# Kernel tuning notes

Measured on AMD Instinct MI355X. Metric: run time of the kernel, lower is better.

## Reference

```python
import jax, jax.numpy as jnp
import numpy as np

# Config constants matching init_kwargs (layer_no=2 -> stride 8, anch_mask=[0,1,2])
ANCHORS = np.array([[10,13],[16,30],[33,23],[30,61],[62,45],[59,119],
                    [116,90],[156,198],[373,326]], np.float32)
STRIDE = 8.0
N_CLASSES = 80
A = 3          # n_anchors in this head
IGNORE = 0.7   # ignore_thre
LAMBDA = 0.5


def _forward(xin, labels, W, b):
    B = xin.shape[0]
    F = xin.shape[2]
    n_ch = 5 + N_CLASSES
    anchors = jnp.asarray(ANCHORS) / STRIDE      # all_anchors_grid, [9,2]
    m_anch = anchors[:A]                         # masked_anchors (anch_mask=[0,1,2])

    # 1x1 conv -> [B, A, F, F, n_ch]
    out = jnp.einsum('bchw,oc->bohw', xin, W) + b[None, :, None, None]
    out = out.reshape(B, A, n_ch, F, F).transpose(0, 1, 3, 4, 2)
    ch = jnp.arange(n_ch)
    output = jnp.where((ch < 2) | (ch >= 4), jax.nn.sigmoid(out), out)

    # box decode (pred); only [..., :4] is used (detached) for IoU ignore mask
    xs = jnp.arange(F, dtype=xin.dtype)
    pred_x = output[..., 0] + xs                 # x varies along last spatial axis
    pred_y = output[..., 1] + xs[:, None]        # y varies along rows
    pred_w = jnp.exp(output[..., 2]) * m_anch[:, 0][None, :, None, None]
    pred_h = jnp.exp(output[..., 3]) * m_anch[:, 1][None, :, None, None]
    pred4 = jax.lax.stop_gradient(jnp.stack([pred_x, pred_y, pred_w, pred_h], -1))

    lab = jax.lax.stop_gradient(labels)          # original uses labels.cpu().data
    valid = lab.sum(-1) > 0                      # [B,K]
    tx = lab[..., 1] * F
    ty = lab[..., 2] * F
    tw = lab[..., 3] * F
    th = lab[..., 4] * F
    ti = tx.astype(jnp.int32)
    tj = ty.astype(jnp.int32)
    tbox = jnp.stack([tx, ty, tw, th], -1)       # [B,K,4]

    # anchor matching: bboxes_iou(truth_box, ref_anchors) with xyxy=True, faithful to source
    ref = jnp.concatenate([jnp.zeros_like(anchors), anchors], -1)   # [9,4] = [0,0,w,h]
    tl = jnp.maximum(tbox[..., None, :2], ref[:, :2])
    br = jnp.minimum(tbox[..., None, 2:], ref[:, 2:])
    area_a = jnp.prod(tbox[..., 2:] - tbox[..., :2], -1)            # [B,K]
    area_b = anchors[:, 0] * anchors[:, 1]                          # [9]
    ai = jnp.prod(br - tl, -1) * jnp.all(tl < br, -1)
    a_iou = ai / (area_a[..., None] + area_b - ai)                  # [B,K,9]
    a_iou = jnp.where(valid[..., None], a_iou, -1.0)
    best_all = jnp.argmax(a_iou, -1)                                # [B,K]
    best_mask = best_all < A                                        # in anch_mask {0,1,2}
    best_n = best_all % A

    # pred-vs-truth IoU (xywh) -> objectness ignore mask
    p = pred4.reshape(B, -1, 4)                                     # [B, A*F*F, 4]
    ptl = p[..., :2] - p[..., 2:] * 0.5
    pbr = p[..., :2] + p[..., 2:] * 0.5
    ttl = tbox[..., :2] - tbox[..., 2:] * 0.5
    tbr = tbox[..., :2] + tbox[..., 2:] * 0.5
    tl2 = jnp.maximum(ptl[:, :, None], ttl[:, None])                # [B,N,K,2]
    br2 = jnp.minimum(pbr[:, :, None], tbr[:, None])
    ai2 = jnp.prod(br2 - tl2, -1) * jnp.all(tl2 < br2, -1)
    denom = (p[..., 2] * p[..., 3])[:, :, None] + (tbox[..., 2] * tbox[..., 3])[:, None, :] - ai2
    piou = jnp.where(valid[:, None, :], ai2 / denom, 0.0)
    obj_mask = 1.0 - (piou.max(-1) > IGNORE).astype(xin.dtype).reshape(B, A, F, F)

    # vectorized scatter of per-truth-box assignments
    assign = valid & best_mask
    bidx = jnp.broadcast_to(jnp.arange(B)[:, None], valid.shape)
    lin = ((bidx * A + best_n) * F + tj) * F + ti
    ncells = B * A * F * F
    lin = jnp.where(assign, lin, ncells).reshape(-1)    # OOB rows dropped in scatter

    aw = m_anch[best_n, 0]
    ah = m_anch[best_n, 1]
    onehot = jax.nn.one_hot(lab[..., 0].astype(jnp.int32), N_CLASSES, dtype=xin.dtype)
    tvec = jnp.concatenate([
        (tx - ti)[..., None], (ty - tj)[..., None],
        jnp.log(tw / aw + 1e-16)[..., None], jnp.log(th / ah + 1e-16)[..., None],
        jnp.ones_like(tx)[..., None], onehot], -1).reshape(-1, n_ch)
    scale = jnp.sqrt(2.0 - tw * th / (F * F))           # [B,K]

    obj_mask = obj_mask.reshape(-1).at[lin].set(1.0, mode='drop').reshape(B, A, F, F)
    tgt_mask = jnp.zeros((ncells, 4 + N_CLASSES), xin.dtype).at[lin].set(1.0, mode='drop')
    tgt_mask = tgt_mask.reshape(B, A, F, F, 4 + N_CLASSES)
    tgt_scale = jnp.zeros((ncells, 2), xin.dtype).at[lin].set(
        jnp.stack([scale, scale], -1).reshape(-1, 2), mode='drop').reshape(B, A, F, F, 2)
    target = jnp.zeros((ncells, n_ch), xin.dtype).at[lin].set(tvec, mode='drop')
    target = target.reshape(B, A, F, F, n_ch)

    def process(x):
        xy = x[..., :2] * tgt_mask[..., :2]
        wh = x[..., 2:4] * tgt_mask[..., 2:4] * tgt_scale
        obj = (x[..., 4] * obj_mask)[..., None]
        cl = x[..., 5:] * tgt_mask[..., 4:]
        return jnp.concatenate([xy, wh, obj, cl], -1)

    o = process(output)
    t = process(target)

    def bce(p_, t_, w=None):
        # torch BCELoss clamps log terms at -100
        l = -(t_ * jnp.maximum(jnp.log(p_), -100.0)
              + (1.0 - t_) * jnp.maximum(jnp.log(1.0 - p_), -100.0))
        return (l * w if w is not None else l).sum()

    loss_xy = bce(o[..., :2], t[..., :2], tgt_scale * tgt_scale)
    loss_wh = LAMBDA * ((o[..., 2:4] - t[..., 2:4]) ** 2).sum()
    loss_obj = bce(o[..., 4], t[..., 4])
    loss_cls = bce(o[..., 5:], t[..., 5:])
    loss_l2 = ((o - t) ** 2).sum()
    loss = loss_xy + loss_wh + loss_obj + loss_cls
    return jnp.stack([loss, loss_xy, loss_wh, loss_obj, loss_cls, loss_l2])


def setup_inputs() -> dict:
    key = jax.random.key(0)
    k1, k2, k3, k4, k5 = jax.random.split(key, 5)
    B, C, F, K = 16, 256, 76, 40
    n_ch = 5 + N_CLASSES
    xin = jax.random.normal(k1, (B, C, F, F), jnp.float32)
    W = jax.random.normal(k2, (A * n_ch, C), jnp.float32) * 0.02  # 1x1 conv weight
    b = jnp.zeros((A * n_ch,), jnp.float32)
    cls = jax.random.randint(k3, (B, K, 1), 0, N_CLASSES).astype(jnp.float32)
    xy = jax.random.uniform(k4, (B, K, 2), jnp.float32, 0.05, 0.95)
    wh = jax.random.uniform(k5, (B, K, 2), jnp.float32, 0.02, 0.4)
    labels = jnp.concatenate([cls, xy, wh], -1)   # [B,K,5] = [class,xc,yc,w,h]
    return {"xin": xin, "labels": labels, "W": W, "b": b}


def reference(xin, labels, W, b):
    return _forward(xin, labels, W, b)
```

## Files before the change

kernel.cpp:

```cpp
#include <hip/hip_runtime.h>
#include <math.h>

typedef unsigned int u32;
typedef unsigned short u16;
typedef __attribute__((ext_vector_type(2))) u32 u32x2;
typedef __attribute__((ext_vector_type(4))) u32 u32x4;
typedef __attribute__((ext_vector_type(8))) short bf16x8;
typedef __attribute__((ext_vector_type(4))) float f32x4;

#define FDIM 76
#define NCELL 5776
#define NA 3
#define NCH 85
#define NCLS 80
#define KLAB 40
#define NB 16
#define CIN 256
#define TILES_PER_B 91
#define NBLK (NB * TILES_PER_B)
#define CS_LD 68

__device__ __forceinline__ float sigmf_(float x) { return __frcp_rn(1.0f + __expf(-x)); }
__device__ __forceinline__ float bce_fullf(float p, float t) {
    return -(t * fmaxf(__logf(p), -100.0f) + (1.0f - t) * fmaxf(__logf(1.0f - p), -100.0f));
}
__device__ __forceinline__ float bce1f(float p) { return -fmaxf(__logf(p), -100.0f); }
__device__ __forceinline__ float bce0f(float p) { return -fmaxf(__logf(1.0f - p), -100.0f); }

__device__ __forceinline__ u16 bf16rne(float f) {
    u32 u = __float_as_uint(f);
    u32 r = u + 0x7fffu + ((u >> 16) & 1u);
    return (u16)(r >> 16);
}
__device__ __forceinline__ float bf16f(u16 v) { return __uint_as_float(((u32)v) << 16); }

__global__ __launch_bounds__(256) void yolo_wconv(const float* __restrict__ W,
                                                  u16* __restrict__ Wbf) {
    int idx = blockIdx.x * 256 + threadIdx.x;
    int row = idx >> 8, col = idx & 255;
    float v = (row < NA * NCH) ? W[row * CIN + col] : 0.0f;
    Wbf[idx] = bf16rne(v);
}

__global__ __launch_bounds__(64) void yolo_lab(const float* __restrict__ labels,
                                               float* __restrict__ lrec) {
    int idx = blockIdx.x * 64 + threadIdx.x;
    if (idx >= NB * KLAB) return;
    const float* l = labels + idx * 5;
    float cls = l[0], x = l[1], y = l[2], ww = l[3], hh = l[4];
    bool valid = (cls + x + y + ww + hh) > 0.0f;
    float tx = x * FDIM, ty = y * FDIM, tw = ww * FDIM, th = hh * FDIM;
    int ti = (int)tx, tj = (int)ty;
    float area_a = (tw - tx) * (th - ty);
    const float aw[9] = {1.25f, 2.0f, 4.125f, 3.75f, 7.75f, 7.375f, 14.5f, 19.5f, 46.625f};
    const float ah[9] = {1.625f, 3.75f, 2.875f, 7.625f, 5.625f, 14.875f, 11.25f, 24.75f, 40.75f};
    float best = -1e30f;
    int bi = 0;
    for (int n = 0; n < 9; n++) {
        float bw = fminf(tw, aw[n]), bh = fminf(th, ah[n]);
        float ai = ((tx < bw) && (ty < bh)) ? (bw - tx) * (bh - ty) : 0.0f;
        float iou = valid ? ai / (area_a + aw[n] * ah[n] - ai) : -1.0f;
        if (iou > best) { best = iou; bi = n; }
    }
    int bn = bi % 3;
    bool assign = valid && (bi < 3);
    float* r = lrec + idx * 16;
    r[0] = tx - 0.5f * tw; r[1] = ty - 0.5f * th;
    r[2] = tx + 0.5f * tw; r[3] = ty + 0.5f * th;
    r[4] = tw * th;
    r[5] = valid ? 1.0f : 0.0f;
    r[6] = assign ? (float)((bn * FDIM + tj) * FDIM + ti) : -1.0f;
    r[7] = sqrtf(2.0f - tw * th / (float)(FDIM * FDIM));
    r[8] = tx - (float)ti; r[9] = ty - (float)tj;
    r[10] = logf(tw / aw[bn] + 1e-16f); r[11] = logf(th / ah[bn] + 1e-16f);
    r[12] = cls; r[13] = 0.0f; r[14] = 0.0f; r[15] = 0.0f;
}

__global__ __launch_bounds__(512, 4) void yolo_mfma(const float* __restrict__ xin,
                                                    const u16* __restrict__ Wbf,
                                                    const float* __restrict__ bias,
                                                    const float* __restrict__ lrec,
                                                    float* __restrict__ partials) {
    __shared__ char smem[34816];
    __shared__ float Lb[KLAB * 16];
    __shared__ float red[8][8];

    u16* Csb = (u16*)smem;

    const int blk = blockIdx.x;
    const int b = blk / TILES_PER_B;
    const int tile = blk - b * TILES_PER_B;
    const int cell0 = tile * 64;
    const int t = threadIdx.x;
    const int lane = t & 63;
    const int wid = t >> 6;
    const int g = lane >> 4;
    const int l15 = lane & 15;

    const float* xbase = xin + (size_t)b * CIN * NCELL;
    float xv[32];
    {
        const int cell = t & 63;
        const int cg0 = cell0 + cell;
        const int cg = cg0 < NCELL ? cg0 : NCELL - 1;
        const int kq0 = (t >> 6);
#pragma unroll
        for (int kc = 0; kc < 4; kc++)
#pragma unroll
            for (int ii = 0; ii < 2; ii++) {
                const int kq = kq0 + ii * 8;
                const float* xp = xbase + (size_t)(kc * 64 + kq * 4) * NCELL + cg;
                xv[kc * 8 + ii * 4 + 0] = xp[0];
                xv[kc * 8 + ii * 4 + 1] = xp[NCELL];
                xv[kc * 8 + ii * 4 + 2] = xp[2 * NCELL];
                xv[kc * 8 + ii * 4 + 3] = xp[3 * NCELL];
            }
    }

    for (int i = t; i < KLAB * 16; i += 512) Lb[i] = lrec[b * KLAB * 16 + i];

    f32x4 acc[2][4];
#pragma unroll
    for (int mi = 0; mi < 2; mi++)
#pragma unroll
        for (int ni = 0; ni < 4; ni++) acc[mi][ni] = (f32x4){0.f, 0.f, 0.f, 0.f};

    const u16* wrow = Wbf + (wid * 32 + l15) * CIN;

#pragma unroll
    for (int kc = 0; kc < 4; kc++) {
        u16* Xs = (u16*)(smem + ((kc & 1) ? 8192 : 0));
        bf16x8 af0[2];
#pragma unroll
        for (int mi = 0; mi < 2; mi++)
            af0[mi] = *(const bf16x8*)(wrow + mi * 16 * CIN + kc * 64 + g * 8);
#pragma unroll
        for (int ii = 0; ii < 2; ii++) {
            const int u = t + ii * 512;
            const int kq = u >> 6, cell = u & 63;
            u32x2 pv;
            pv.x = (u32)bf16rne(xv[kc * 8 + ii * 4 + 0]) | ((u32)bf16rne(xv[kc * 8 + ii * 4 + 1]) << 16);
            pv.y = (u32)bf16rne(xv[kc * 8 + ii * 4 + 2]) | ((u32)bf16rne(xv[kc * 8 + ii * 4 + 3]) << 16);
            const int byte = (cell * 128 + kq * 8) ^ ((cell & 7) << 4);
            *(u32x2*)((char*)Xs + byte) = pv;
        }
        __syncthreads();
        bf16x8 bfr[4];
#pragma unroll
        for (int ni = 0; ni < 4; ni++) {
            const int cell = ni * 16 + l15;
            const int byte = (cell * 128 + g * 16) ^ ((cell & 7) << 4);
            bfr[ni] = *(const bf16x8*)((char*)Xs + byte);
        }
        bf16x8 af1[2];
#pragma unroll
        for (int mi = 0; mi < 2; mi++)
            af1[mi] = *(const bf16x8*)(wrow + mi * 16 * CIN + kc * 64 + 32 + g * 8);
#pragma unroll
        for (int mi = 0; mi < 2; mi++)
#pragma unroll
            for (int ni = 0; ni < 4; ni++)
                acc[mi][ni] = __builtin_amdgcn_mfma_f32_16x16x32_bf16(
                    af0[mi], bfr[ni], acc[mi][ni], 0, 0, 0);
#pragma unroll
        for (int ni = 0; ni < 4; ni++) {
            const int cell = ni * 16 + l15;
            const int byte = (cell * 128 + 64 + g * 16) ^ ((cell & 7) << 4);
            bfr[ni] = *(const bf16x8*)((char*)Xs + byte);
        }
#pragma unroll
        for (int mi = 0; mi < 2; mi++)
#pragma unroll
            for (int ni = 0; ni < 4; ni++)
                acc[mi][ni] = __builtin_amdgcn_mfma_f32_16x16x32_bf16(
                    af1[mi], bfr[ni], acc[mi][ni], 0, 0, 0);
    }

    __syncthreads();

    float bv[8];
#pragma unroll
    for (int mi = 0; mi < 2; mi++)
#pragma unroll
        for (int reg = 0; reg < 4; reg++) {
            const int ch = wid * 32 + mi * 16 + g * 4 + reg;
            bv[mi * 4 + reg] = (ch < NA * NCH) ? bias[ch] : 0.0f;
        }
#pragma unroll
    for (int mi = 0; mi < 2; mi++)
#pragma unroll
        for (int ni = 0; ni < 4; ni++)
#pragma unroll
            for (int reg = 0; reg < 4; reg++) {
                const int ch = wid * 32 + mi * 16 + g * 4 + reg;
                const int cell = ni * 16 + l15;
                Csb[ch * CS_LD + cell] = bf16rne(acc[mi][ni][reg] + bv[mi * 4 + reg]);
            }
    __syncthreads();

    float part[5] = {0.f, 0.f, 0.f, 0.f, 0.f};
    if (t < 384) {
        const int half = (t >= 192) ? 1 : 0;
        const int unit = t - half * 192;
        const int a = unit >> 6;
        const int c = unit & 63;
        const int cg = cell0 + c;
        if (cg < NCELL) {
            const int chb = a * NCH;
            const int hh = cg / FDIM;
            const int ww = cg - hh * FDIM;
            const float mykey = (float)((a * FDIM + hh) * FDIM + ww);
            if (half == 0) {
                float v0 = bf16f(Csb[(chb + 0) * CS_LD + c]);
                float v1 = bf16f(Csb[(chb + 1) * CS_LD + c]);
                float v2 = bf16f(Csb[(chb + 2) * CS_LD + c]);
                float v3 = bf16f(Csb[(chb + 3) * CS_LD + c]);
                float v4 = bf16f(Csb[(chb + 4) * CS_LD + c]);
                const float manw[3] = {1.25f, 2.0f, 4.125f};
                const float manh[3] = {1.625f, 3.75f, 2.875f};
                float s0 = sigmf_(v0), s1 = sigmf_(v1), s4 = sigmf_(v4);
                float pw = __expf(v2) * manw[a];
                float ph = __expf(v3) * manh[a];
                float px = s0 + (float)ww, py = s1 + (float)hh;
                float parea = pw * ph;
                float ptlx = px - 0.5f * pw, ptly = py - 0.5f * ph;
                float pbrx = px + 0.5f * pw, pbry = py + 0.5f * ph;

                float maxiou = -1e30f;
                int aidx = -1;
                for (int k = 0; k < KLAB; k++) {
                    const f32x4 A = *(const f32x4*)&Lb[k * 16];
                    const f32x4 Bq = *(const f32x4*)&Lb[k * 16 + 4];
                    float tlx = fmaxf(ptlx, A.x), tly = fmaxf(ptly, A.y);
                    float brx = fminf(pbrx, A.z), bry = fminf(pbry, A.w);
                    float inter = ((tlx < brx) && (tly < bry)) ? (brx - tlx) * (bry - tly) : 0.0f;
                    float iou = (Bq.y != 0.0f) ? inter * __frcp_rn(parea + Bq.x - inter) : 0.0f;
                    maxiou = fmaxf(maxiou, iou);
                    if (Bq.z == mykey) aidx = k;
                }
                if (aidx >= 0) {
                    const f32x4 Bq = *(const f32x4*)&Lb[aidx * 16 + 4];
                    const f32x4 Tv = *(const f32x4*)&Lb[aidx * 16 + 8];
                    float sc = Bq.w, sc2 = sc * sc;
                    part[0] += sc2 * (bce_fullf(s0, Tv.x) + bce_fullf(s1, Tv.y));
                    float dw = v2 - Tv.z, dh = v3 - Tv.w;
                    float whq = dw * dw + dh * dh;
                    part[1] += 0.5f * sc2 * whq;
                    part[2] += bce1f(s4);
                    int ci = (int)Lb[aidx * 16 + 12];
                    float l2 = (s0 - Tv.x) * (s0 - Tv.x) + (s1 - Tv.y) * (s1 - Tv.y) +
                               sc2 * whq + (s4 - 1.0f) * (s4 - 1.0f);
                    float lcls = 0.0f;
                    for (int cc = 0; cc < 40; cc++) {
                        float s = sigmf_(bf16f(Csb[(chb + 5 + cc) * CS_LD + c]));
                        if (cc == ci) { lcls += bce1f(s); l2 += (s - 1.0f) * (s - 1.0f); }
                        else          { lcls += bce0f(s); l2 += s * s; }
                    }
                    part[3] += lcls;
                    part[4] += l2;
                } else {
                    bool objm = !(maxiou > 0.7f);
                    if (objm) { part[2] += bce0f(s4); part[4] += s4 * s4; }
                }
            } else {
                int aidx = -1;
                for (int k = 0; k < KLAB; k++) {
                    const f32x4 Bq = *(const f32x4*)&Lb[k * 16 + 4];
                    if (Bq.z == mykey) aidx = k;
                }
                if (aidx >= 0) {
                    int ci = (int)Lb[aidx * 16 + 12];
                    float lcls = 0.0f, l2 = 0.0f;
                    for (int cc = 40; cc < 80; cc++) {
                        float s = sigmf_(bf16f(Csb[(chb + 5 + cc) * CS_LD + c]));
                        if (cc == ci) { lcls += bce1f(s); l2 += (s - 1.0f) * (s - 1.0f); }
                        else          { lcls += bce0f(s); l2 += s * s; }
                    }
                    part[3] += lcls;
                    part[4] += l2;
                }
            }
        }
    }

#pragma unroll
    for (int i = 0; i < 5; i++) {
        float v = part[i];
        for (int off = 32; off > 0; off >>= 1) v += __shfl_down(v, off);
        if ((t & 63) == 0) red[t >> 6][i] = v;
    }
    __syncthreads();
    if (t == 0) {
        float s[5];
#pragma unroll
        for (int i = 0; i < 5; i++) {
            s[i] = red[0][i];
#pragma unroll
            for (int wv = 1; wv < 8; wv++) s[i] += red[wv][i];
            partials[blk * 8 + i] = s[i];
        }
    }
}

__global__ __launch_bounds__(256) void yolo_fin(const float* __restrict__ partials,
                                                float* __restrict__ out) {
    __shared__ float red[4][8];
    const int t = threadIdx.x;
    float s[5] = {0.f, 0.f, 0.f, 0.f, 0.f};
    for (int r = t; r < NBLK; r += 256)
#pragma unroll
        for (int i = 0; i < 5; i++) s[i] += partials[r * 8 + i];
#pragma unroll
    for (int i = 0; i < 5; i++) {
        float v = s[i];
        for (int off = 32; off > 0; off >>= 1) v += __shfl_down(v, off);
        if ((t & 63) == 0) red[t >> 6][i] = v;
    }
    __syncthreads();
    if (t == 0) {
        float xy  = red[0][0] + red[1][0] + red[2][0] + red[3][0];
        float wh  = red[0][1] + red[1][1] + red[2][1] + red[3][1];
        float obj = red[0][2] + red[1][2] + red[2][2] + red[3][2];
        float cls = red[0][3] + red[1][3] + red[2][3] + red[3][3];
        float l2  = red[0][4] + red[1][4] + red[2][4] + red[3][4];
        out[0] = xy + wh + obj + cls;
        out[1] = xy; out[2] = wh; out[3] = obj; out[4] = cls; out[5] = l2;
    }
}

extern "C" void kernel_launch(void* const* d_in, const int* in_sizes, int n_in,
                              void* d_out, int out_size, void* d_ws, size_t ws_size,
                              hipStream_t stream) {
    const float* xin    = (const float*)d_in[0];
    const float* labels = (const float*)d_in[1];
    const float* Wm     = (const float*)d_in[2];
    const float* bias   = (const float*)d_in[3];
    float* out = (float*)d_out;

    float* partials = (float*)d_ws;
    float* lrec  = (float*)((char*)d_ws + 46592);
    u16*   Wbf   = (u16*)((char*)d_ws + 46592 + 40960);

    yolo_wconv<<<256, 256, 0, stream>>>(Wm, Wbf);
    yolo_lab<<<(NB * KLAB + 63) / 64, 64, 0, stream>>>(labels, lrec);
    yolo_mfma<<<NBLK, 512, 0, stream>>>(xin, Wbf, bias, lrec, partials);
    yolo_fin<<<1, 256, 0, stream>>>(partials, out);
}
```

Measured before the change: 86.38 us.

## Split fused GEMM+loss kernel into separate GEMM and loss kernels via global bf16 buffer

Splits the previously fused conv-GEMM-plus-loss kernel into a GEMM kernel that writes bf16 conv outputs to a global workspace buffer and a separate loss kernel where one thread handles each anchor-cell. The aim is to remove load imbalance and the idle threads in the fused epilogue, where only 384 of 512 threads worked and the IoU and label scan serialized behind the GEMM. Global x loads now happen per k-chunk instead of all up front, which lowers register pressure. In exchange it adds about 47 MB of extra global write and read traffic plus an extra launch. The fused kernel is kept as a fallback when the workspace is too small.

Result: slower. 105.4 us (+22.0%).

```diff
diff --git a/kernel.cpp b/kernel.cpp
--- a/kernel.cpp
+++ b/kernel.cpp
@@ -18,6 +18,8 @@
 #define CIN 256
 #define TILES_PER_B 91
 #define NBLK (NB * TILES_PER_B)
+#define LOSS_BLKX 68
+#define NBLK2 (NB * LOSS_BLKX)
 #define CS_LD 68
 
 __device__ __forceinline__ float sigmf_(float x) { return __frcp_rn(1.0f + __expf(-x)); }
@@ -76,14 +78,11 @@
     r[12] = cls; r[13] = 0.0f; r[14] = 0.0f; r[15] = 0.0f;
 }
 
-__global__ __launch_bounds__(512, 4) void yolo_mfma(const float* __restrict__ xin,
+__global__ __launch_bounds__(512, 4) void yolo_gemm(const float* __restrict__ xin,
                                                     const u16* __restrict__ Wbf,
                                                     const float* __restrict__ bias,
-                                                    const float* __restrict__ lrec,
-                                                    float* __restrict__ partials) {
+                                                    u16* __restrict__ Cg) {
     __shared__ char smem[34816];
-    __shared__ float Lb[KLAB * 16];
-    __shared__ float red[8][8];
 
     u16* Csb = (u16*)smem;
 
@@ -97,34 +96,13 @@
     const int g = lane >> 4;
     const int l15 = lane & 15;
 
+    f32x4 acc[2][4];
+#pragma unroll
+    for (int mi = 0; mi < 2; mi++)
+#pragma unroll
+        for (int ni = 0; ni < 4; ni++) acc[mi][ni] = (f32x4){0.f, 0.f, 0.f, 0.f};
+
     const float* xbase = xin + (size_t)b * CIN * NCELL;
-    float xv[32];
-    {
-        const int cell = t & 63;
-        const int cg0 = cell0 + cell;
-        const int cg = cg0 < NCELL ? cg0 : NCELL - 1;
-        const int kq0 = (t >> 6);
-#pragma unroll
-        for (int kc = 0; kc < 4; kc++)
-#pragma unroll
-            for (int ii = 0; ii < 2; ii++) {
-                const int kq = kq0 + ii * 8;
-                const float* xp = xbase + (size_t)(kc * 64 + kq * 4) * NCELL + cg;
-                xv[kc * 8 + ii * 4 + 0] = xp[0];
-                xv[kc * 8 + ii * 4 + 1] = xp[NCELL];
-                xv[kc * 8 + ii * 4 + 2] = xp[2 * NCELL];
-                xv[kc * 8 + ii * 4 + 3] = xp[3 * NCELL];
-            }
-    }
-
-    for (int i = t; i < KLAB * 16; i += 512) Lb[i] = lrec[b * KLAB * 16 + i];
-
-    f32x4 acc[2][4];
-#pragma unroll
-    for (int mi = 0; mi < 2; mi++)
-#pragma unroll
-        for (int ni = 0; ni < 4; ni++) acc[mi][ni] = (f32x4){0.f, 0.f, 0.f, 0.f};
-
     const u16* wrow = Wbf + (wid * 32 + l15) * CIN;
 
 #pragma unroll
@@ -134,13 +112,26 @@
 #pragma unroll
         for (int mi = 0; mi < 2; mi++)
             af0[mi] = *(const bf16x8*)(wrow + mi * 16 * CIN + kc * 64 + g * 8);
+        float xv[8];
+#pragma unroll
+        for (int ii = 0; ii < 2; ii++) {
+            const int u = t + ii * 512;
+            const int kq = u >> 6, cell = u & 63;
+            const int cg0 = cell0 + cell;
+            const int cg = cg0 < NCELL ? cg0 : NCELL - 1;
+            const float* xp = xbase + (size_t)(kc * 64 + kq * 4) * NCELL + cg;
+            xv[ii * 4 + 0] = xp[0];
+            xv[ii * 4 + 1] = xp[NCELL];
+            xv[ii * 4 + 2] = xp[2 * NCELL];
+            xv[ii * 4 + 3] = xp[3 * NCELL];
+        }
 #pragma unroll
         for (int ii = 0; ii < 2; ii++) {
             const int u = t + ii * 512;
             const int kq = u >> 6, cell = u & 63;
             u32x2 pv;
-            pv.x = (u32)bf16rne(xv[kc * 8 + ii * 4 + 0]) | ((u32)bf16rne(xv[kc * 8 + ii * 4 + 1]) << 16);
-            pv.y = (u32)bf16rne(xv[kc * 8 + ii * 4 + 2]) | ((u32)bf16rne(xv[kc * 8 + ii * 4 + 3]) << 16);
+            pv.x = (u32)bf16rne(xv[ii * 4 + 0]) | ((u32)bf16rne(xv[ii * 4 + 1]) << 16);
+            pv.y = (u32)bf16rne(xv[ii * 4 + 2]) | ((u32)bf16rne(xv[ii * 4 + 3]) << 16);
             const int byte = (cell * 128 + kq * 8) ^ ((cell & 7) << 4);
             *(u32x2*)((char*)Xs + byte) = pv;
         }
@@ -198,6 +189,216 @@
             }
     __syncthreads();
 
+    u16* cgb = Cg + (size_t)b * 256 * NCELL;
+#pragma unroll
+    for (int it = 0; it < 16; it++) {
+        const int i = t + it * 512;
+        const int ch = i >> 5;
+        const int cw = i & 31;
+        const int cell = cell0 + cw * 2;
+        if (cell + 2 <= NCELL) {
+            u32 v = *(const u32*)&Csb[ch * CS_LD + cw * 2];
+            *(u32*)&cgb[(size_t)ch * NCELL + cell] = v;
+        }
+    }
+}
+
+__global__ __launch_bounds__(256) void yolo_loss(const u16* __restrict__ Cg,
+                                                 const float* __restrict__ lrec,
+                                                 float* __restrict__ partials) {
+    __shared__ float Lb[KLAB * 16];
+    __shared__ float red[4][8];
+    const int b = blockIdx.y;
+    const int t = threadIdx.x;
+    const int idx = blockIdx.x * 256 + t;
+
+    for (int i = t; i < KLAB * 16; i += 256) Lb[i] = lrec[b * KLAB * 16 + i];
+    __syncthreads();
+
+    float part[5] = {0.f, 0.f, 0.f, 0.f, 0.f};
+    if (idx < NA * NCELL) {
+        int a = 0, cell = idx;
+        if (idx >= 2 * NCELL)      { a = 2; cell = idx - 2 * NCELL; }
+        else if (idx >= NCELL)     { a = 1; cell = idx - NCELL; }
+        const int hh = cell / FDIM;
+        const int ww = cell - hh * FDIM;
+        const float mykey = (float)((a * FDIM + hh) * FDIM + ww);
+        const u16* cp = Cg + (size_t)b * 256 * NCELL + (size_t)(a * NCH) * NCELL + cell;
+
+        float v0 = bf16f(cp[0]);
+        float v1 = bf16f(cp[NCELL]);
+        float v2 = bf16f(cp[2 * NCELL]);
+        float v3 = bf16f(cp[3 * NCELL]);
+        float v4 = bf16f(cp[4 * NCELL]);
+        const float manw[3] = {1.25f, 2.0f, 4.125f};
+        const float manh[3] = {1.625f, 3.75f, 2.875f};
+        float s0 = sigmf_(v0), s1 = sigmf_(v1), s4 = sigmf_(v4);
+        float pw = __expf(v2) * manw[a];
+        float ph = __expf(v3) * manh[a];
+        float px = s0 + (float)ww, py = s1 + (float)hh;
+        float parea = pw * ph;
+        float ptlx = px - 0.5f * pw, ptly = py - 0.5f * ph;
+        float pbrx = px + 0.5f * pw, pbry = py + 0.5f * ph;
+
+        float maxiou = -1e30f;
+        int aidx = -1;
+        for (int k = 0; k < KLAB; k++) {
+            const f32x4 A  = *(const f32x4*)&Lb[k * 16];
+            const f32x4 Bq = *(const f32x4*)&Lb[k * 16 + 4];
+            float tlx = fmaxf(ptlx, A.x), tly = fmaxf(ptly, A.y);
+            float brx = fminf(pbrx, A.z), bry = fminf(pbry, A.w);
+            float inter = ((tlx < brx) && (tly < bry)) ? (brx - tlx) * (bry - tly) : 0.0f;
+            float iou = (Bq.y != 0.0f) ? inter * __frcp_rn(parea + Bq.x - inter) : 0.0f;
+            maxiou = fmaxf(maxiou, iou);
+            if (Bq.z == mykey) aidx = k;
+        }
+        if (aidx >= 0) {
+            const f32x4 Bq = *(const f32x4*)&Lb[aidx * 16 + 4];
+            const f32x4 Tv = *(const f32x4*)&Lb[aidx * 16 + 8];
+            float sc = Bq.w, sc2 = sc * sc;
+            part[0] += sc2 * (bce_fullf(s0, Tv.x) + bce_fullf(s1, Tv.y));
+            float dw = v2 - Tv.z, dh = v3 - Tv.w;
+            float whq = dw * dw + dh * dh;
+            part[1] += 0.5f * sc2 * whq;
+            part[2] += bce1f(s4);
+            int ci = (int)Lb[aidx * 16 + 12];
+            float l2 = (s0 - Tv.x) * (s0 - Tv.x) + (s1 - Tv.y) * (s1 - Tv.y) +
+                       sc2 * whq + (s4 - 1.0f) * (s4 - 1.0f);
+            float lcls = 0.0f;
+#pragma unroll 4
+            for (int cc = 0; cc < NCLS; cc++) {
+                float s = sigmf_(bf16f(cp[(size_t)(5 + cc) * NCELL]));
+                if (cc == ci) { lcls += bce1f(s); l2 += (s - 1.0f) * (s - 1.0f); }
+                else          { lcls += bce0f(s); l2 += s * s; }
+            }
+            part[3] += lcls;
+            part[4] += l2;
+        } else {
+            bool objm = !(maxiou > 0.7f);
+            if (objm) { part[2] += bce0f(s4); part[4] += s4 * s4; }
+        }
+    }
+
+#pragma unroll
+    for (int i = 0; i < 5; i++) {
+        float v = part[i];
+        for (int off = 32; off > 0; off >>= 1) v += __shfl_down(v, off);
+        if ((t & 63) == 0) red[t >> 6][i] = v;
+    }
+    __syncthreads();
+    if (t == 0) {
+#pragma unroll
+        for (int i = 0; i < 5; i++)
+            partials[(b * LOSS_BLKX + blockIdx.x) * 8 + i] =
+                red[0][i] + red[1][i] + red[2][i] + red[3][i];
+    }
+}
+
+__global__ __launch_bounds__(512, 4) void yolo_mfma(const float* __restrict__ xin,
+                                                    const u16* __restrict__ Wbf,
+                                                    const float* __restrict__ bias,
+                                                    const float* __restrict__ lrec,
+                                                    float* __restrict__ partials) {
+    __shared__ char smem[34816];
+    __shared__ float Lb[KLAB * 16];
+    __shared__ float red[8][8];
+    u16* Csb = (u16*)smem;
+    const int blk = blockIdx.x;
+    const int b = blk / TILES_PER_B;
+    const int tile = blk - b * TILES_PER_B;
+    const int cell0 = tile * 64;
+    const int t = threadIdx.x;
+    const int lane = t & 63;
+    const int wid = t >> 6;
+    const int g = lane >> 4;
+    const int l15 = lane & 15;
+
+    for (int i = t; i < KLAB * 16; i += 512) Lb[i] = lrec[b * KLAB * 16 + i];
+
+    f32x4 acc[2][4];
+#pragma unroll
+    for (int mi = 0; mi < 2; mi++)
+#pragma unroll
+        for (int ni = 0; ni < 4; ni++) acc[mi][ni] = (f32x4){0.f, 0.f, 0.f, 0.f};
+    const float* xbase = xin + (size_t)b * CIN * NCELL;
+    const u16* wrow = Wbf + (wid * 32 + l15) * CIN;
+#pragma unroll
+    for (int kc = 0; kc < 4; kc++) {
+        u16* Xs = (u16*)(smem + ((kc & 1) ? 8192 : 0));
+        bf16x8 af0[2];
+#pragma unroll
+        for (int mi = 0; mi < 2; mi++)
+            af0[mi] = *(const bf16x8*)(wrow + mi * 16 * CIN + kc * 64 + g * 8);
+        float xv[8];
+#pragma unroll
+        for (int ii = 0; ii < 2; ii++) {
+            const int u = t + ii * 512;
+            const int kq = u >> 6, cell = u & 63;
+            const int cg0 = cell0 + cell;
+            const int cg = cg0 < NCELL ? cg0 : NCELL - 1;
+            const float* xp = xbase + (size_t)(kc * 64 + kq * 4) * NCELL + cg;
+            xv[ii * 4 + 0] = xp[0]; xv[ii * 4 + 1] = xp[NCELL];
+            xv[ii * 4 + 2] = xp[2 * NCELL]; xv[ii * 4 + 3] = xp[3 * NCELL];
+        }
+#pragma unroll
+        for (int ii = 0; ii < 2; ii++) {
+            const int u = t + ii * 512;
+            const int kq = u >> 6, cell = u & 63;
+            u32x2 pv;
+            pv.x = (u32)bf16rne(xv[ii * 4 + 0]) | ((u32)bf16rne(xv[ii * 4 + 1]) << 16);
+            pv.y = (u32)bf16rne(xv[ii * 4 + 2]) | ((u32)bf16rne(xv[ii * 4 + 3]) << 16);
+            const int byte = (cell * 128 + kq * 8) ^ ((cell & 7) << 4);
+            *(u32x2*)((char*)Xs + byte) = pv;
+        }
+        __syncthreads();
+        bf16x8 bfr[4];
+#pragma unroll
+        for (int ni = 0; ni < 4; ni++) {
+            const int cell = ni * 16 + l15;
+            const int byte = (cell * 128 + g * 16) ^ ((cell & 7) << 4);
+            bfr[ni] = *(const bf16x8*)((char*)Xs + byte);
+        }
+        bf16x8 af1[2];
+#pragma unroll
+        for (int mi = 0; mi < 2; mi++)
+            af1[mi] = *(const bf16x8*)(wrow + mi * 16 * CIN + kc * 64 + 32 + g * 8);
+#pragma unroll
+        for (int mi = 0; mi < 2; mi++)
+#pragma unroll
+            for (int ni = 0; ni < 4; ni++)
+                acc[mi][ni] = __builtin_amdgcn_mfma_f32_16x16x32_bf16(af0[mi], bfr[ni], acc[mi][ni], 0, 0, 0);
+#pragma unroll
+        for (int ni = 0; ni < 4; ni++) {
+            const int cell = ni * 16 + l15;
+            const int byte = (cell * 128 + 64 + g * 16) ^ ((cell & 7) << 4);
+            bfr[ni] = *(const bf16x8*)((char*)Xs + byte);
+        }
+#pragma unroll
+        for (int mi = 0; mi < 2; mi++)
+#pragma unroll
+            for (int ni = 0; ni < 4; ni++)
+                acc[mi][ni] = __builtin_amdgcn_mfma_f32_16x16x32_bf16(af1[mi], bfr[ni], acc[mi][ni], 0, 0, 0);
+    }
+    __syncthreads();
+    float bv[8];
+#pragma unroll
+    for (int mi = 0; mi < 2; mi++)
+#pragma unroll
+        for (int reg = 0; reg < 4; reg++) {
+            const int ch = wid * 32 + mi * 16 + g * 4 + reg;
+            bv[mi * 4 + reg] = (ch < NA * NCH) ? bias[ch] : 0.0f;
+        }
+#pragma unroll
+    for (int mi = 0; mi < 2; mi++)
+#pragma unroll
+        for (int ni = 0; ni < 4; ni++)
+#pragma unroll
+            for (int reg = 0; reg < 4; reg++) {
+                const int ch = wid * 32 + mi * 16 + g * 4 + reg;
+                const int cell = ni * 16 + l15;
+                Csb[ch * CS_LD + cell] = bf16rne(acc[mi][ni][reg] + bv[mi * 4 + reg]);
+            }
+    __syncthreads();
     float part[5] = {0.f, 0.f, 0.f, 0.f, 0.f};
     if (t < 384) {
         const int half = (t >= 192) ? 1 : 0;
@@ -225,7 +426,6 @@
                 float parea = pw * ph;
                 float ptlx = px - 0.5f * pw, ptly = py - 0.5f * ph;
                 float pbrx = px + 0.5f * pw, pbry = py + 0.5f * ph;
-
                 float maxiou = -1e30f;
                 int aidx = -1;
                 for (int k = 0; k < KLAB; k++) {
@@ -256,8 +456,7 @@
                         if (cc == ci) { lcls += bce1f(s); l2 += (s - 1.0f) * (s - 1.0f); }
                         else          { lcls += bce0f(s); l2 += s * s; }
                     }
-                    part[3] += lcls;
-                    part[4] += l2;
+                    part[3] += lcls; part[4] += l2;
                 } else {
                     bool objm = !(maxiou > 0.7f);
                     if (objm) { part[2] += bce0f(s4); part[4] += s4 * s4; }
@@ -276,13 +475,11 @@
                         if (cc == ci) { lcls += bce1f(s); l2 += (s - 1.0f) * (s - 1.0f); }
                         else          { lcls += bce0f(s); l2 += s * s; }
                     }
-                    part[3] += lcls;
-                    part[4] += l2;
+                    part[3] += lcls; part[4] += l2;
                 }
             }
         }
     }
-
 #pragma unroll
     for (int i = 0; i < 5; i++) {
         float v = part[i];
@@ -303,11 +500,11 @@
 }
 
 __global__ __launch_bounds__(256) void yolo_fin(const float* __restrict__ partials,
-                                                float* __restrict__ out) {
+                                                float* __restrict__ out, int n) {
     __shared__ float red[4][8];
     const int t = threadIdx.x;
     float s[5] = {0.f, 0.f, 0.f, 0.f, 0.f};
-    for (int r = t; r < NBLK; r += 256)
+    for (int r = t; r < n; r += 256)
 #pragma unroll
         for (int i = 0; i < 5; i++) s[i] += partials[r * 8 + i];
 #pragma unroll
@@ -340,9 +537,17 @@
     float* partials = (float*)d_ws;
     float* lrec  = (float*)((char*)d_ws + 46592);
     u16*   Wbf   = (u16*)((char*)d_ws + 46592 + 40960);
+    u16*   Cg    = (u16*)((char*)d_ws + 218624);
+    const size_t NEEDED = 218624ull + (size_t)NB * 256 * NCELL * 2;
 
     yolo_wconv<<<256, 256, 0, stream>>>(Wm, Wbf);
     yolo_lab<<<(NB * KLAB + 63) / 64, 64, 0, stream>>>(labels, lrec);
-    yolo_mfma<<<NBLK, 512, 0, stream>>>(xin, Wbf, bias, lrec, partials);
-    yolo_fin<<<1, 256, 0, stream>>>(partials, out);
-}
+    if (ws_size >= NEEDED) {
+        yolo_gemm<<<NBLK, 512, 0, stream>>>(xin, Wbf, bias, Cg);
+        yolo_loss<<<dim3(LOSS_BLKX, NB), 256, 0, stream>>>(Cg, lrec, partials);
+        yolo_fin<<<1, 256, 0, stream>>>(partials, out, NBLK2);
+    } else {
+        yolo_mfma<<<NBLK, 512, 0, stream>>>(xin, Wbf, bias, lrec, partials);
+        yolo_fin<<<1, 256, 0, stream>>>(partials, out, NBLK);
+    }
+}
```

## Stage fp32 input tile into LDS via direct global-to-LDS loads

Applied to the files above, without the earlier changes.

Replaces the register-staged load of the 256x64 fp32 input tile (later packed to bf16 in LDS) with async global_load_lds transfers that write the whole fp32 tile straight into a 64 KB swizzled LDS buffer. Each MFMA B-fragment is then built by reading eight fp32 values from LDS and rounding them to bf16, and the per-k-chunk barriers are dropped. This cuts register pressure and avoids a VGPR round trip. In exchange, LDS use per block roughly doubles, which limits occupancy with 512-thread blocks, and the scalar LDS reads plus per-element conversion inside the MFMA loop add instruction overhead.

Result: slower. 90.38 us (+4.6%).

```diff
diff --git a/kernel.cpp b/kernel.cpp
--- a/kernel.cpp
+++ b/kernel.cpp
@@ -4,7 +4,6 @@
 typedef unsigned int u32;
 typedef unsigned short u16;
 typedef __attribute__((ext_vector_type(2))) u32 u32x2;
-typedef __attribute__((ext_vector_type(4))) u32 u32x4;
 typedef __attribute__((ext_vector_type(8))) short bf16x8;
 typedef __attribute__((ext_vector_type(4))) float f32x4;
 
@@ -19,6 +18,9 @@
 #define TILES_PER_B 91
 #define NBLK (NB * TILES_PER_B)
 #define CS_LD 68
+
+typedef __attribute__((address_space(1))) const void gvoid_t;
+typedef __attribute__((address_space(3))) void svoid_t;
 
 __device__ __forceinline__ float sigmf_(float x) { return __frcp_rn(1.0f + __expf(-x)); }
 __device__ __forceinline__ float bce_fullf(float p, float t) {
@@ -81,11 +83,11 @@
                                                     const float* __restrict__ bias,
                                                     const float* __restrict__ lrec,
                                                     float* __restrict__ partials) {
-    __shared__ char smem[34816];
-    __shared__ float Lb[KLAB * 16];
-    __shared__ float red[8][8];
-
-    u16* Csb = (u16*)smem;
+    __shared__ char smem[68608];
+    float* Xf  = (float*)smem;
+    u16*  Csb  = (u16*)smem;
+    float* Lb  = (float*)(smem + 65536);
+    float* red = (float*)(smem + 68096);
 
     const int blk = blockIdx.x;
     const int b = blk / TILES_PER_B;
@@ -98,82 +100,54 @@
     const int l15 = lane & 15;
 
     const float* xbase = xin + (size_t)b * CIN * NCELL;
-    float xv[32];
-    {
-        const int cell = t & 63;
-        const int cg0 = cell0 + cell;
-        const int cg = cg0 < NCELL ? cg0 : NCELL - 1;
-        const int kq0 = (t >> 6);
-#pragma unroll
-        for (int kc = 0; kc < 4; kc++)
-#pragma unroll
-            for (int ii = 0; ii < 2; ii++) {
-                const int kq = kq0 + ii * 8;
-                const float* xp = xbase + (size_t)(kc * 64 + kq * 4) * NCELL + cg;
-                xv[kc * 8 + ii * 4 + 0] = xp[0];
-                xv[kc * 8 + ii * 4 + 1] = xp[NCELL];
-                xv[kc * 8 + ii * 4 + 2] = xp[2 * NCELL];
-                xv[kc * 8 + ii * 4 + 3] = xp[3 * NCELL];
+#pragma unroll
+    for (int i = 0; i < 32; i++) {
+        const int p = wid * 32 + i;
+        const int sw = ((p >> 3) & 3) << 4;
+        const int cl = cell0 + (lane ^ sw);
+        const int cg = cl < NCELL ? cl : NCELL - 1;
+        __builtin_amdgcn_global_load_lds(
+            (gvoid_t*)(xbase + (size_t)p * NCELL + cg),
+            (svoid_t*)(Xf + p * 64), 4, 0, 0);
+    }
+
+    for (int i = t; i < KLAB * 16; i += 512) Lb[i] = lrec[b * KLAB * 16 + i];
+
+    f32x4 acc[2][4];
+#pragma unroll
+    for (int mi = 0; mi < 2; mi++)
+#pragma unroll
+        for (int ni = 0; ni < 4; ni++) acc[mi][ni] = (f32x4){0.f, 0.f, 0.f, 0.f};
+
+    const u16* wrow = Wbf + (wid * 32 + l15) * CIN;
+
+    __syncthreads();
+
+#pragma unroll
+    for (int kc = 0; kc < 4; kc++) {
+#pragma unroll
+        for (int s = 0; s < 2; s++) {
+            const int k0 = kc * 64 + s * 32 + g * 8;
+            const int sw = ((k0 >> 3) & 3) << 4;
+            bf16x8 a0 = *(const bf16x8*)(wrow + 0 * 16 * CIN + kc * 64 + s * 32 + g * 8);
+            bf16x8 a1 = *(const bf16x8*)(wrow + 1 * 16 * CIN + kc * 64 + s * 32 + g * 8);
+#pragma unroll
+            for (int ni = 0; ni < 4; ni++) {
+                const int cidx = (ni * 16 + l15) ^ sw;
+                const float* xp = Xf + k0 * 64 + cidx;
+                bf16x8 bfr;
+                bfr[0] = (short)bf16rne(xp[0 * 64]);
+                bfr[1] = (short)bf16rne(xp[1 * 64]);
+                bfr[2] = (short)bf16rne(xp[2 * 64]);
+                bfr[3] = (short)bf16rne(xp[3 * 64]);
+                bfr[4] = (short)bf16rne(xp[4 * 64]);
+                bfr[5] = (short)bf16rne(xp[5 * 64]);
+                bfr[6] = (short)bf16rne(xp[6 * 64]);
+                bfr[7] = (short)bf16rne(xp[7 * 64]);
+                acc[0][ni] = __builtin_amdgcn_mfma_f32_16x16x32_bf16(a0, bfr, acc[0][ni], 0, 0, 0);
+                acc[1][ni] = __builtin_amdgcn_mfma_f32_16x16x32_bf16(a1, bfr, acc[1][ni], 0, 0, 0);
             }
-    }
-
-    for (int i = t; i < KLAB * 16; i += 512) Lb[i] = lrec[b * KLAB * 16 + i];
-
-    f32x4 acc[2][4];
-#pragma unroll
-    for (int mi = 0; mi < 2; mi++)
-#pragma unroll
-        for (int ni = 0; ni < 4; ni++) acc[mi][ni] = (f32x4){0.f, 0.f, 0.f, 0.f};
-
-    const u16* wrow = Wbf + (wid * 32 + l15) * CIN;
-
-#pragma unroll
-    for (int kc = 0; kc < 4; kc++) {
-        u16* Xs = (u16*)(smem + ((kc & 1) ? 8192 : 0));
-        bf16x8 af0[2];
-#pragma unroll
-        for (int mi = 0; mi < 2; mi++)
-            af0[mi] = *(const bf16x8*)(wrow + mi * 16 * CIN + kc * 64 + g * 8);
-#pragma unroll
-        for (int ii = 0; ii < 2; ii++) {
-            const int u = t + ii * 512;
-            const int kq = u >> 6, cell = u & 63;
-            u32x2 pv;
-            pv.x = (u32)bf16rne(xv[kc * 8 + ii * 4 + 0]) | ((u32)bf16rne(xv[kc * 8 + ii * 4 + 1]) << 16);
-            pv.y = (u32)bf16rne(xv[kc * 8 + ii * 4 + 2]) | ((u32)bf16rne(xv[kc * 8 + ii * 4 + 3]) << 16);
-            const int byte = (cell * 128 + kq * 8) ^ ((cell & 7) << 4);
-            *(u32x2*)((char*)Xs + byte) = pv;
         }
-        __syncthreads();
-        bf16x8 bfr[4];
-#pragma unroll
-        for (int ni = 0; ni < 4; ni++) {
-            const int cell = ni * 16 + l15;
-            const int byte = (cell * 128 + g * 16) ^ ((cell & 7) << 4);
-            bfr[ni] = *(const bf16x8*)((char*)Xs + byte);
-        }
-        bf16x8 af1[2];
-#pragma unroll
-        for (int mi = 0; mi < 2; mi++)
-            af1[mi] = *(const bf16x8*)(wrow + mi * 16 * CIN + kc * 64 + 32 + g * 8);
-#pragma unroll
-        for (int mi = 0; mi < 2; mi++)
-#pragma unroll
-            for (int ni = 0; ni < 4; ni++)
-                acc[mi][ni] = __builtin_amdgcn_mfma_f32_16x16x32_bf16(
-                    af0[mi], bfr[ni], acc[mi][ni], 0, 0, 0);
-#pragma unroll
-        for (int ni = 0; ni < 4; ni++) {
-            const int cell = ni * 16 + l15;
-            const int byte = (cell * 128 + 64 + g * 16) ^ ((cell & 7) << 4);
-            bfr[ni] = *(const bf16x8*)((char*)Xs + byte);
-        }
-#pragma unroll
-        for (int mi = 0; mi < 2; mi++)
-#pragma unroll
-            for (int ni = 0; ni < 4; ni++)
-                acc[mi][ni] = __builtin_amdgcn_mfma_f32_16x16x32_bf16(
-                    af1[mi], bfr[ni], acc[mi][ni], 0, 0, 0);
     }
 
     __syncthreads();
@@ -225,11 +199,10 @@
                 float parea = pw * ph;
                 float ptlx = px - 0.5f * pw, ptly = py - 0.5f * ph;
                 float pbrx = px + 0.5f * pw, pbry = py + 0.5f * ph;
-
                 float maxiou = -1e30f;
                 int aidx = -1;
                 for (int k = 0; k < KLAB; k++) {
-                    const f32x4 A = *(const f32x4*)&Lb[k * 16];
+                    const f32x4 A  = *(const f32x4*)&Lb[k * 16];
                     const f32x4 Bq = *(const f32x4*)&Lb[k * 16 + 4];
                     float tlx = fmaxf(ptlx, A.x), tly = fmaxf(ptly, A.y);
                     float brx = fminf(pbrx, A.z), bry = fminf(pbry, A.w);
@@ -256,8 +229,7 @@
                         if (cc == ci) { lcls += bce1f(s); l2 += (s - 1.0f) * (s - 1.0f); }
                         else          { lcls += bce0f(s); l2 += s * s; }
                     }
-                    part[3] += lcls;
-                    part[4] += l2;
+                    part[3] += lcls; part[4] += l2;
                 } else {
                     bool objm = !(maxiou > 0.7f);
                     if (objm) { part[2] += bce0f(s4); part[4] += s4 * s4; }
@@ -276,8 +248,7 @@
                         if (cc == ci) { lcls += bce1f(s); l2 += (s - 1.0f) * (s - 1.0f); }
                         else          { lcls += bce0f(s); l2 += s * s; }
                     }
-                    part[3] += lcls;
-                    part[4] += l2;
+                    part[3] += lcls; part[4] += l2;
                 }
             }
         }
@@ -287,27 +258,26 @@
     for (int i = 0; i < 5; i++) {
         float v = part[i];
         for (int off = 32; off > 0; off >>= 1) v += __shfl_down(v, off);
-        if ((t & 63) == 0) red[t >> 6][i] = v;
+        if ((t & 63) == 0) red[(t >> 6) * 8 + i] = v;
     }
     __syncthreads();
     if (t == 0) {
-        float s[5];
 #pragma unroll
         for (int i = 0; i < 5; i++) {
-            s[i] = red[0][i];
-#pragma unroll
-            for (int wv = 1; wv < 8; wv++) s[i] += red[wv][i];
-            partials[blk * 8 + i] = s[i];
+            float s = red[i];
+#pragma unroll
+            for (int wv = 1; wv < 8; wv++) s += red[wv * 8 + i];
+            partials[blk * 8 + i] = s;
         }
     }
 }
 
 __global__ __launch_bounds__(256) void yolo_fin(const float* __restrict__ partials,
-                                                float* __restrict__ out) {
+                                                float* __restrict__ out, int n) {
     __shared__ float red[4][8];
     const int t = threadIdx.x;
     float s[5] = {0.f, 0.f, 0.f, 0.f, 0.f};
-    for (int r = t; r < NBLK; r += 256)
+    for (int r = t; r < n; r += 256)
 #pragma unroll
         for (int i = 0; i < 5; i++) s[i] += partials[r * 8 + i];
 #pragma unroll
@@ -344,5 +314,5 @@
     yolo_wconv<<<256, 256, 0, stream>>>(Wm, Wbf);
     yolo_lab<<<(NB * KLAB + 63) / 64, 64, 0, stream>>>(labels, lrec);
     yolo_mfma<<<NBLK, 512, 0, stream>>>(xin, Wbf, bias, lrec, partials);
-    yolo_fin<<<1, 256, 0, stream>>>(partials, out);
-}
+    yolo_fin<<<1, 256, 0, stream>>>(partials, out, NBLK);
+}
```
